# Kernel optimization log

Hardware: AMD Instinct MI355X
Metric: run time of the kernel (lower is better)

The kernel has to match this reference:

```python
import jax, jax.numpy as jnp
import numpy as np

NUM_CODES = 8192
LATENT_DIM = 256
BETA = 0.25
EPS_NORM = 1e-12  # F.normalize eps


def setup_inputs() -> dict:
    key = jax.random.key(0)
    k1, k2 = jax.random.split(key)
    z = jax.random.normal(k1, (8, LATENT_DIM, 32, 32), dtype=jnp.float32)
    # embedding initialized uniform(-1/K, 1/K); use that scale for realism
    codebook = jax.random.uniform(k2, (NUM_CODES, LATENT_DIM), dtype=jnp.float32,
                                  minval=-1.0 / NUM_CODES, maxval=1.0 / NUM_CODES)
    return {"z": z, "codebook": codebook}


def reference(z, codebook):
    # forward re-normalizes the codebook rows (F.normalize dim=1)
    norm = jnp.sqrt(jnp.sum(codebook * codebook, axis=1, keepdims=True))
    w = codebook / jnp.maximum(norm, EPS_NORM)                      # [K, D]

    z_perm = jnp.transpose(z, (0, 2, 3, 1))                          # [B, H, W, D]
    B, H, W, D = z_perm.shape
    zf = z_perm.reshape(-1, D)                                       # [N, D]

    # squared euclidean distances: ||z||^2 + ||w||^2 - 2 z w^T
    d = (jnp.sum(zf * zf, axis=1, keepdims=True)
         + jnp.sum(w * w, axis=1)
         - 2.0 * jnp.einsum('nd,kd->nk', zf, w))                     # [N, K]
    idx = jnp.argmin(d, axis=1)                                      # [N] int

    z_q = w[idx].reshape(B, H, W, D)                                 # gather

    # commitment + codebook loss
    loss = (jnp.mean((jax.lax.stop_gradient(z_q) - z_perm) ** 2)
            + BETA * jnp.mean((z_q - jax.lax.stop_gradient(z_perm)) ** 2))

    # straight-through estimator
    z_q = z_perm + jax.lax.stop_gradient(z_q - z_perm)

    # perplexity from codeword usage histogram (== mean of one-hots)
    N = idx.shape[0]
    counts = jnp.zeros((NUM_CODES,), dtype=jnp.float32).at[idx].add(1.0)
    avg_probs = counts / N
    perplexity = jnp.exp(-jnp.sum(avg_probs * jnp.log(avg_probs + 1e-10)))

    z_q = jnp.transpose(z_q, (0, 3, 1, 2))                           # back to NCHW
    return (z_q, idx, loss, perplexity)
```

## Files before the change

kernel.cpp:

```cpp
#include <hip/hip_runtime.h>
#include <hip/hip_bf16.h>
#include <math.h>

#define KC 8192
#define DD 256
#define NP 8192
#define ZQ_ELEMS 2097152
#define MARGIN_S 2.5e-4f
#define NPART 32

#define OFF_ABIG 0u
#define OFF_BBIG 8388608u
#define OFF_NRM  16777216u
#define OFF_WSQ  16809984u
#define OFF_ZSQ  16842752u
#define OFF_PV1  16875520u
#define OFF_PV2  17924096u
#define OFF_PK1  18972672u
#define OFF_LOSSP 20021248u
#define OFF_IDX  20025344u
#define OFF_FLAG 20058112u
#define OFF_HIST 20090880u
#define OFF_PACK 20123648u
#define OFF_LIST 20189184u
#define OFF_NFLG 20221952u

typedef __attribute__((ext_vector_type(8))) short bf16x8;
typedef __attribute__((ext_vector_type(4))) float f32x4;
typedef __attribute__((address_space(3))) void as3_void;
typedef const __attribute__((address_space(1))) void as1_cvoid;

#define GLOAD16(g, l) __builtin_amdgcn_global_load_lds((as1_cvoid*)(g), (as3_void*)(l), 16, 0, 0)

__device__ inline double waveReduceD(double v) {
#pragma unroll
    for (int off = 32; off; off >>= 1) v += __shfl_down(v, off, 64);
    return v;
}

static __device__ inline unsigned short f2bf(float f) {
    __hip_bfloat16 h = __float2bfloat16(f);
    return *(unsigned short*)&h;
}
static __device__ inline float bf2f(unsigned short u) {
    unsigned v = ((unsigned)u) << 16;
    float f;
    __builtin_memcpy(&f, &v, 4);
    return f;
}

__global__ __launch_bounds__(256) void prep(
    const float* __restrict__ cb, const float* __restrict__ z,
    unsigned short* __restrict__ Bbig, unsigned short* __restrict__ Abig,
    float* __restrict__ nrm, float* __restrict__ wsq, float* __restrict__ zsq,
    int* __restrict__ hist, int* __restrict__ nflag) {
    __shared__ double lred[4];
    __shared__ float mh;
    int bid = blockIdx.x, t = threadIdx.x;
    int lane = t & 63, wid = t >> 6;
    if (bid < KC) {
        int k = bid;
        if (k < 32) hist[k * 256 + t] = 0;
        if (k == 32 && t == 0) *nflag = 0;
        float c = cb[k * DD + t];
        double s = waveReduceD((double)c * (double)c);
        if (lane == 0) lred[wid] = s;
        __syncthreads();
        if (t == 0) {
            double tot = lred[0] + lred[1] + lred[2] + lred[3];
            float nf = sqrtf((float)tot);
            mh = fmaxf(nf, 1e-12f);
        }
        __syncthreads();
        float wv = c / mh;
        unsigned short hi = f2bf(wv);
        unsigned short lo = f2bf(wv - bf2f(hi));
        Bbig[k * 512 + t] = hi;
        Bbig[k * 512 + 256 + t] = lo;
        if (t == 0) nrm[k] = mh;
        __syncthreads();
        double s2 = waveReduceD((double)wv * (double)wv);
        if (lane == 0) lred[wid] = s2;
        __syncthreads();
        if (t == 0) wsq[k] = (float)(lred[0] + lred[1] + lred[2] + lred[3]);
    } else {
        int n = bid - KC;
        int b = n >> 10, hw = n & 1023;
        float v = z[(b * DD + t) * 1024 + hw];
        unsigned short hi = f2bf(v);
        unsigned short lo = f2bf(v - bf2f(hi));
        Abig[n * 512 + t] = hi;
        Abig[n * 512 + 256 + t] = lo;
        double s = waveReduceD((double)v * (double)v);
        if (lane == 0) lred[wid] = s;
        __syncthreads();
        if (t == 0) zsq[n] = (float)(lred[0] + lred[1] + lred[2] + lred[3]);
    }
}

__global__ __launch_bounds__(512, 2) void gemm_top2(
    const unsigned short* __restrict__ Abig, const unsigned short* __restrict__ Bbig,
    const float* __restrict__ wsq,
    float* __restrict__ pv1, float* __restrict__ pv2, int* __restrict__ pk1) {
    __shared__ unsigned short sAB[65536];

    int t = threadIdx.x;
    int l = t & 63, w = t >> 6;
    int wm = w >> 2, wn = w & 3;
    int kc0 = blockIdx.y * 256;
    int n0 = blockIdx.x * 256;

    int row0 = t >> 2;
    int lsw = (((t & 3) ^ ((row0 >> 1) & 3)) << 3);
    int subsw = (((l >> 4) ^ ((l >> 1) & 3)) << 3);

#define STAGE(kt_) do {                                                        \
    int p_ = (kt_) >> 3;                                                       \
    int zo_ = (p_ == 2 ? 256 : 0) + ((kt_) & 7) * 32;                          \
    int wo_ = (p_ == 1 ? 256 : 0) + ((kt_) & 7) * 32;                          \
    int b_ = ((kt_) & 3) * 16384;                                              \
    GLOAD16(Bbig + (size_t)(kc0 + row0) * 512 + wo_ + lsw, &sAB[b_ + t * 8]);  \
    GLOAD16(Bbig + (size_t)(kc0 + row0 + 128) * 512 + wo_ + lsw, &sAB[b_ + 4096 + t * 8]); \
    GLOAD16(Abig + (size_t)(n0 + row0) * 512 + zo_ + lsw, &sAB[b_ + 8192 + t * 8]); \
    GLOAD16(Abig + (size_t)(n0 + row0 + 128) * 512 + zo_ + lsw, &sAB[b_ + 12288 + t * 8]); \
} while (0)

    f32x4 acc[8][4];
#pragma unroll
    for (int mf = 0; mf < 8; ++mf) {
#pragma unroll
        for (int r = 0; r < 4; ++r) {
            float hv = -0.5f * wsq[kc0 + wm * 128 + mf * 16 + ((l >> 4) << 2) + r];
#pragma unroll
            for (int nf = 0; nf < 4; ++nf) acc[mf][nf][r] = hv;
        }
    }

#define KBODY(bufbase) do {                                                    \
    bf16x8 af[8], bfr[4];                                                      \
    _Pragma("unroll")                                                          \
    for (int mf = 0; mf < 8; ++mf)                                             \
        af[mf] = *(const bf16x8*)&sAB[(bufbase) + (wm * 128 + mf * 16 + (l & 15)) * 32 + subsw]; \
    _Pragma("unroll")                                                          \
    for (int nf = 0; nf < 4; ++nf)                                             \
        bfr[nf] = *(const bf16x8*)&sAB[(bufbase) + 8192 + (wn * 64 + nf * 16 + (l & 15)) * 32 + subsw]; \
    __builtin_amdgcn_s_setprio(1);                                             \
    _Pragma("unroll")                                                          \
    for (int mf = 0; mf < 8; ++mf)                                             \
        _Pragma("unroll")                                                      \
        for (int nf = 0; nf < 4; ++nf)                                         \
            acc[mf][nf] = __builtin_amdgcn_mfma_f32_16x16x32_bf16(af[mf], bfr[nf], acc[mf][nf], 0, 0, 0); \
    __builtin_amdgcn_s_setprio(0);                                             \
} while (0)

    STAGE(0);
    STAGE(1);
    STAGE(2);
    asm volatile("s_waitcnt vmcnt(8)" ::: "memory");
    __builtin_amdgcn_s_barrier();
    asm volatile("" ::: "memory");

    for (int kt = 0; kt < 21; ++kt) {
        STAGE(kt + 3);
        KBODY((kt & 3) * 16384);
        asm volatile("s_waitcnt vmcnt(8)" ::: "memory");
        __builtin_amdgcn_s_barrier();
        asm volatile("" ::: "memory");
    }
    KBODY(1 * 16384);
    asm volatile("s_waitcnt vmcnt(4)" ::: "memory");
    __builtin_amdgcn_s_barrier();
    asm volatile("" ::: "memory");
    KBODY(2 * 16384);
    asm volatile("s_waitcnt vmcnt(0)" ::: "memory");
    __builtin_amdgcn_s_barrier();
    asm volatile("" ::: "memory");
    KBODY(3 * 16384);

    float v1[4], v2[4];
    int k1[4];
#pragma unroll
    for (int nf = 0; nf < 4; ++nf) { v1[nf] = 3.4e38f; v2[nf] = 3.4e38f; k1[nf] = 0; }
#pragma unroll
    for (int mf = 0; mf < 8; ++mf) {
#pragma unroll
        for (int r = 0; r < 4; ++r) {
            int code = kc0 + wm * 128 + mf * 16 + ((l >> 4) << 2) + r;
#pragma unroll
            for (int nf = 0; nf < 4; ++nf) {
                float dv = -acc[mf][nf][r];
                bool lt = dv < v1[nf];
                v2[nf] = fminf(v2[nf], fmaxf(v1[nf], dv));
                v1[nf] = fminf(v1[nf], dv);
                k1[nf] = lt ? code : k1[nf];
            }
        }
    }
#pragma unroll
    for (int nf = 0; nf < 4; ++nf) {
#pragma unroll
        for (int mask = 16; mask <= 32; mask <<= 1) {
            float ov1 = __shfl_xor(v1[nf], mask, 64);
            float ov2 = __shfl_xor(v2[nf], mask, 64);
            int ok1 = __shfl_xor(k1[nf], mask, 64);
            bool take = (ov1 < v1[nf]) || (ov1 == v1[nf] && ok1 < k1[nf]);
            if (take) { v2[nf] = fminf(v1[nf], ov2); v1[nf] = ov1; k1[nf] = ok1; }
            else v2[nf] = fminf(v2[nf], ov1);
        }
    }
    __syncthreads();
    float* sv1 = (float*)sAB;
    float* sv2 = sv1 + 512;
    int* sk1 = (int*)(sv2 + 512);
    if ((l >> 4) == 0) {
#pragma unroll
        for (int nf = 0; nf < 4; ++nf) {
            int col = wn * 64 + nf * 16 + l;
            sv1[col * 2 + wm] = v1[nf];
            sv2[col * 2 + wm] = v2[nf];
            sk1[col * 2 + wm] = k1[nf];
        }
    }
    __syncthreads();
    if (t < 256) {
        float a1 = sv1[t * 2], b1 = sv1[t * 2 + 1];
        float a2 = sv2[t * 2], b2 = sv2[t * 2 + 1];
        int ak = sk1[t * 2], bk = sk1[t * 2 + 1];
        bool tb = (b1 < a1) || (b1 == a1 && bk < ak);
        float w1 = tb ? b1 : a1;
        int wk = tb ? bk : ak;
        float w2 = tb ? fminf(b2, a1) : fminf(a2, b1);
        pv1[blockIdx.y * NP + n0 + t] = w1;
        pv2[blockIdx.y * NP + n0 + t] = w2;
        pk1[blockIdx.y * NP + n0 + t] = wk;
    }
#undef STAGE
#undef KBODY
}

__global__ __launch_bounds__(256) void merge_top2(
    const float* __restrict__ pv1, const float* __restrict__ pv2,
    const int* __restrict__ pk1, int* __restrict__ idxw, int* __restrict__ flag,
    int* __restrict__ list, int* __restrict__ nflag,
    unsigned long long* __restrict__ packed) {
    int n = blockIdx.x * 256 + threadIdx.x;
    float gv1 = 3.4e38f, gv2 = 3.4e38f;
    int gk1 = 0;
#pragma unroll
    for (int ct = 0; ct < NPART; ++ct) {
        float v1 = pv1[ct * NP + n];
        if (v1 < gv1) {
            gv2 = fminf(gv1, pv2[ct * NP + n]);
            gv1 = v1;
            gk1 = pk1[ct * NP + n];
        } else {
            gv2 = fminf(gv2, v1);
        }
    }
    idxw[n] = gk1;
    int f = (gv2 - gv1 < MARGIN_S) ? 1 : 0;
    flag[n] = f;
    if (f) {
        packed[n] = 0xFFFFFFFFFFFFFFFFull;
        int pos = atomicAdd(nflag, 1);
        list[pos] = n;
    }
}

__global__ __launch_bounds__(256) void rescore_par(
    const float* __restrict__ z, const float* __restrict__ cb,
    const float* __restrict__ nrm, const float* __restrict__ wsq,
    const float* __restrict__ zsq, const int* __restrict__ list,
    const int* __restrict__ nflag, unsigned long long* __restrict__ packed) {
    __shared__ float sz[256];
    int nf = *nflag;
    int t = threadIdx.x;
    int lane = t & 63, wv = t >> 6;
    for (int ii = blockIdx.x; ii < nf; ii += 64) {
        int n = list[ii];
        int b = n >> 10, hw = n & 1023;
        __syncthreads();
        sz[t] = z[(b * DD + t) * 1024 + hw];
        __syncthreads();
        float4 zr = ((const float4*)sz)[lane];
        float zq = zsq[n];
        unsigned long long best = 0xFFFFFFFFFFFFFFFFull;
        int kbase = blockIdx.y * 256 + wv * 64;
        for (int j = 0; j < 64; ++j) {
            int k = kbase + j;
            float4 cc = *(const float4*)&cb[(size_t)k * DD + lane * 4];
            float p = (zr.x * cc.x + zr.y * cc.y) + (zr.z * cc.z + zr.w * cc.w);
#pragma unroll
            for (int off = 32; off; off >>= 1) p += __shfl_xor(p, off, 64);
            float dot = p / nrm[k];
            float dv = (zq + wsq[k]) - 2.0f * dot;
            unsigned bits = __float_as_uint(dv);
            bits = (bits & 0x80000000u) ? ~bits : (bits | 0x80000000u);
            unsigned long long pk = ((unsigned long long)bits << 32) | (unsigned)k;
            best = best < pk ? best : pk;
        }
        if (lane == 0) atomicMin(packed + n, best);
    }
}

__global__ __launch_bounds__(256) void fix_hist(
    const int* __restrict__ flag, const unsigned long long* __restrict__ packed,
    int* __restrict__ idxw, float* __restrict__ out, int* __restrict__ hist) {
    int n = blockIdx.x * 256 + threadIdx.x;
    int k = flag[n] ? (int)(packed[n] & 0xFFFFFFFFull) : idxw[n];
    idxw[n] = k;
    out[ZQ_ELEMS + n] = (float)k;
    atomicAdd(&hist[k], 1);
}

__global__ __launch_bounds__(256) void gather_loss(
    const float* __restrict__ z, const float* __restrict__ cb,
    const float* __restrict__ nrm, const int* __restrict__ idxw,
    float* __restrict__ out, double* __restrict__ lossp) {
    __shared__ double lred[4];
    int t = threadIdx.x;
    int base = (blockIdx.x * 256 + t) * 16;
    double s = 0.0;
#pragma unroll
    for (int q = 0; q < 4; ++q) {
        int e = base + q * 4;
        int b = e >> 18, d = (e >> 10) & 255, hw = e & 1023;
        int n = (b << 10) + hw;
        float4 zv = *(const float4*)&z[e];
        float o[4];
#pragma unroll
        for (int j = 0; j < 4; ++j) {
            int k = idxw[n + j];
            o[j] = cb[k * DD + d] / nrm[k];
        }
        *(float4*)&out[e] = make_float4(o[0], o[1], o[2], o[3]);
        float d0 = o[0] - zv.x, d1 = o[1] - zv.y, d2 = o[2] - zv.z, d3 = o[3] - zv.w;
        s += (double)(d0 * d0) + (double)(d1 * d1) + (double)(d2 * d2) + (double)(d3 * d3);
    }
    s = waveReduceD(s);
    int lane = t & 63, wid = t >> 6;
    if (lane == 0) lred[wid] = s;
    __syncthreads();
    if (t == 0) lossp[blockIdx.x] = lred[0] + lred[1] + lred[2] + lred[3];
}

__global__ __launch_bounds__(256) void finalize_kernel(
    const int* __restrict__ hist, const double* __restrict__ lossp,
    float* __restrict__ out) {
    __shared__ double lred[4];
    __shared__ double lsum;
    int t = threadIdx.x;
    int lane = t & 63, wid = t >> 6;
    double ls = lossp[t] + lossp[t + 256];
    ls = waveReduceD(ls);
    if (lane == 0) lred[wid] = ls;
    __syncthreads();
    if (t == 0) lsum = lred[0] + lred[1] + lred[2] + lred[3];
    __syncthreads();
    double s = 0.0;
    for (int i = t; i < KC; i += 256) {
        float p = (float)hist[i] * (1.0f / 8192.0f);
        float lg = logf(p + 1e-10f);
        s += (double)(p * lg);
    }
    s = waveReduceD(s);
    if (lane == 0) lred[wid] = s;
    __syncthreads();
    if (t == 0) {
        double tot = lred[0] + lred[1] + lred[2] + lred[3];
        float m = (float)(lsum / (double)ZQ_ELEMS);
        out[ZQ_ELEMS + NP] = m + 0.25f * m;
        out[ZQ_ELEMS + NP + 1] = expf(-(float)tot);
    }
}

extern "C" void kernel_launch(void* const* d_in, const int* in_sizes, int n_in,
                              void* d_out, int out_size, void* d_ws, size_t ws_size,
                              hipStream_t stream) {
    const float* z = (const float*)d_in[0];
    const float* cb = (const float*)d_in[1];
    float* out = (float*)d_out;
    char* ws = (char*)d_ws;

    unsigned short* Abig = (unsigned short*)(ws + OFF_ABIG);
    unsigned short* Bbig = (unsigned short*)(ws + OFF_BBIG);
    float* nrm = (float*)(ws + OFF_NRM);
    float* wsq = (float*)(ws + OFF_WSQ);
    float* zsq = (float*)(ws + OFF_ZSQ);
    float* pv1 = (float*)(ws + OFF_PV1);
    float* pv2 = (float*)(ws + OFF_PV2);
    int* pk1 = (int*)(ws + OFF_PK1);
    int* idxw = (int*)(ws + OFF_IDX);
    int* flag = (int*)(ws + OFF_FLAG);
    int* hist = (int*)(ws + OFF_HIST);
    double* lossp = (double*)(ws + OFF_LOSSP);
    unsigned long long* packed = (unsigned long long*)(ws + OFF_PACK);
    int* list = (int*)(ws + OFF_LIST);
    int* nflag = (int*)(ws + OFF_NFLG);

    prep<<<2 * KC, 256, 0, stream>>>(cb, z, Bbig, Abig, nrm, wsq, zsq, hist, nflag);
    gemm_top2<<<dim3(32, NPART), 512, 0, stream>>>(Abig, Bbig, wsq, pv1, pv2, pk1);
    merge_top2<<<NP / 256, 256, 0, stream>>>(pv1, pv2, pk1, idxw, flag, list, nflag, packed);
    rescore_par<<<dim3(64, 32), 256, 0, stream>>>(z, cb, nrm, wsq, zsq, list, nflag, packed);
    fix_hist<<<NP / 256, 256, 0, stream>>>(flag, packed, idxw, out, hist);
    gather_loss<<<ZQ_ELEMS / (256 * 16), 256, 0, stream>>>(z, cb, nrm, idxw, out, lossp);
    finalize_kernel<<<1, 256, 0, stream>>>(hist, lossp, out);
}
```

Measured before the change: 217.4 us.

## Switch GEMM to 32x32x16 MFMA, drop fix_hist kernel, simplify prep reductions

The GEMM moves from 16x16x32 to 32x32x16 bf16 MFMA tiles with a new LDS swizzle, which cuts LDS fragment reads per MFMA and simplifies the top-2 cross-lane reduction. The fix_hist kernel is removed: merge_top2 writes the final index into the packed array, and gather_loss emits the indices and histogram atomics. Prep no longer does a second reduction for wsq (it is derived from the norm) and no longer computes zsq, which rescore now computes on the fly. This saves a launch and some reduction passes, but wsq now comes from tot/mh² rather than an explicit sum, which could shift values slightly.

```diff
diff --git a/kernel.cpp b/kernel.cpp
--- a/kernel.cpp
+++ b/kernel.cpp
@@ -13,20 +13,17 @@
 #define OFF_BBIG 8388608u
 #define OFF_NRM  16777216u
 #define OFF_WSQ  16809984u
-#define OFF_ZSQ  16842752u
 #define OFF_PV1  16875520u
 #define OFF_PV2  17924096u
 #define OFF_PK1  18972672u
 #define OFF_LOSSP 20021248u
-#define OFF_IDX  20025344u
-#define OFF_FLAG 20058112u
 #define OFF_HIST 20090880u
 #define OFF_PACK 20123648u
 #define OFF_LIST 20189184u
 #define OFF_NFLG 20221952u
 
 typedef __attribute__((ext_vector_type(8))) short bf16x8;
-typedef __attribute__((ext_vector_type(4))) float f32x4;
+typedef __attribute__((ext_vector_type(16))) float f32x16;
 typedef __attribute__((address_space(3))) void as3_void;
 typedef const __attribute__((address_space(1))) void as1_cvoid;
 
@@ -52,7 +49,7 @@
 __global__ __launch_bounds__(256) void prep(
     const float* __restrict__ cb, const float* __restrict__ z,
     unsigned short* __restrict__ Bbig, unsigned short* __restrict__ Abig,
-    float* __restrict__ nrm, float* __restrict__ wsq, float* __restrict__ zsq,
+    float* __restrict__ nrm, float* __restrict__ wsq,
     int* __restrict__ hist, int* __restrict__ nflag) {
     __shared__ double lred[4];
     __shared__ float mh;
@@ -70,6 +67,8 @@
             double tot = lred[0] + lred[1] + lred[2] + lred[3];
             float nf = sqrtf((float)tot);
             mh = fmaxf(nf, 1e-12f);
+            nrm[k] = mh;
+            wsq[k] = (float)(tot / ((double)mh * (double)mh));
         }
         __syncthreads();
         float wv = c / mh;
@@ -77,12 +76,6 @@
         unsigned short lo = f2bf(wv - bf2f(hi));
         Bbig[k * 512 + t] = hi;
         Bbig[k * 512 + 256 + t] = lo;
-        if (t == 0) nrm[k] = mh;
-        __syncthreads();
-        double s2 = waveReduceD((double)wv * (double)wv);
-        if (lane == 0) lred[wid] = s2;
-        __syncthreads();
-        if (t == 0) wsq[k] = (float)(lred[0] + lred[1] + lred[2] + lred[3]);
     } else {
         int n = bid - KC;
         int b = n >> 10, hw = n & 1023;
@@ -91,10 +84,6 @@
         unsigned short lo = f2bf(v - bf2f(hi));
         Abig[n * 512 + t] = hi;
         Abig[n * 512 + 256 + t] = lo;
-        double s = waveReduceD((double)v * (double)v);
-        if (lane == 0) lred[wid] = s;
-        __syncthreads();
-        if (t == 0) zsq[n] = (float)(lred[0] + lred[1] + lred[2] + lred[3]);
     }
 }
 
@@ -107,61 +96,77 @@
     int t = threadIdx.x;
     int l = t & 63, w = t >> 6;
     int wm = w >> 2, wn = w & 3;
+    int l31 = l & 31, lhi = l >> 5;
     int kc0 = blockIdx.y * 256;
     int n0 = blockIdx.x * 256;
 
     int row0 = t >> 2;
-    int lsw = (((t & 3) ^ ((row0 >> 1) & 3)) << 3);
-    int subsw = (((l >> 4) ^ ((l >> 1) & 3)) << 3);
-
-#define STAGE(kt_) do {                                                        \
+    int fr = ((row0 >> 1) ^ (row0 >> 3)) & 3;
+    int kk = (((t & 3) ^ fr) << 3);
+    int flr = ((l31 >> 1) ^ (l31 >> 3)) & 3;
+
+#define STAGE4(kt_) do {                                                       \
     int p_ = (kt_) >> 3;                                                       \
     int zo_ = (p_ == 2 ? 256 : 0) + ((kt_) & 7) * 32;                          \
     int wo_ = (p_ == 1 ? 256 : 0) + ((kt_) & 7) * 32;                          \
     int b_ = ((kt_) & 3) * 16384;                                              \
-    GLOAD16(Bbig + (size_t)(kc0 + row0) * 512 + wo_ + lsw, &sAB[b_ + t * 8]);  \
-    GLOAD16(Bbig + (size_t)(kc0 + row0 + 128) * 512 + wo_ + lsw, &sAB[b_ + 4096 + t * 8]); \
-    GLOAD16(Abig + (size_t)(n0 + row0) * 512 + zo_ + lsw, &sAB[b_ + 8192 + t * 8]); \
-    GLOAD16(Abig + (size_t)(n0 + row0 + 128) * 512 + zo_ + lsw, &sAB[b_ + 12288 + t * 8]); \
+    GLOAD16(Bbig + (size_t)(kc0 + row0) * 512 + wo_ + kk, &sAB[b_ + t * 8]);   \
+    GLOAD16(Bbig + (size_t)(kc0 + row0 + 128) * 512 + wo_ + kk, &sAB[b_ + 4096 + t * 8]); \
+    GLOAD16(Abig + (size_t)(n0 + row0) * 512 + zo_ + kk, &sAB[b_ + 8192 + t * 8]); \
+    GLOAD16(Abig + (size_t)(n0 + row0 + 128) * 512 + zo_ + kk, &sAB[b_ + 12288 + t * 8]); \
 } while (0)
 
-    f32x4 acc[8][4];
-#pragma unroll
-    for (int mf = 0; mf < 8; ++mf) {
-#pragma unroll
-        for (int r = 0; r < 4; ++r) {
-            float hv = -0.5f * wsq[kc0 + wm * 128 + mf * 16 + ((l >> 4) << 2) + r];
-#pragma unroll
-            for (int nf = 0; nf < 4; ++nf) acc[mf][nf][r] = hv;
-        }
-    }
-
-#define KBODY(bufbase) do {                                                    \
-    bf16x8 af[8], bfr[4];                                                      \
+    f32x16 acc[4][2];
+#pragma unroll
+    for (int mt = 0; mt < 4; ++mt) {
+#pragma unroll
+        for (int r = 0; r < 16; ++r) {
+            float hv = -0.5f * wsq[kc0 + wm * 128 + mt * 32 + (r & 3) + 8 * (r >> 2) + 4 * lhi];
+            acc[mt][0][r] = hv;
+            acc[mt][1][r] = hv;
+        }
+    }
+
+    int aoff0 = (((0 + lhi) ^ flr) << 3);
+    int aoff1 = (((2 + lhi) ^ flr) << 3);
+
+#define KBODY(bb_) do {                                                        \
+    bf16x8 a0_[4], a1_[4], b0_[2], b1_[2];                                     \
     _Pragma("unroll")                                                          \
-    for (int mf = 0; mf < 8; ++mf)                                             \
-        af[mf] = *(const bf16x8*)&sAB[(bufbase) + (wm * 128 + mf * 16 + (l & 15)) * 32 + subsw]; \
+    for (int mt = 0; mt < 4; ++mt) {                                           \
+        int rb_ = (bb_) + (wm * 128 + mt * 32 + l31) * 32;                     \
+        a0_[mt] = *(const bf16x8*)&sAB[rb_ + aoff0];                           \
+        a1_[mt] = *(const bf16x8*)&sAB[rb_ + aoff1];                           \
+    }                                                                          \
     _Pragma("unroll")                                                          \
-    for (int nf = 0; nf < 4; ++nf)                                             \
-        bfr[nf] = *(const bf16x8*)&sAB[(bufbase) + 8192 + (wn * 64 + nf * 16 + (l & 15)) * 32 + subsw]; \
+    for (int nt = 0; nt < 2; ++nt) {                                           \
+        int rb_ = (bb_) + 8192 + (wn * 64 + nt * 32 + l31) * 32;               \
+        b0_[nt] = *(const bf16x8*)&sAB[rb_ + aoff0];                           \
+        b1_[nt] = *(const bf16x8*)&sAB[rb_ + aoff1];                           \
+    }                                                                          \
     __builtin_amdgcn_s_setprio(1);                                             \
     _Pragma("unroll")                                                          \
-    for (int mf = 0; mf < 8; ++mf)                                             \
+    for (int mt = 0; mt < 4; ++mt)                                             \
         _Pragma("unroll")                                                      \
-        for (int nf = 0; nf < 4; ++nf)                                         \
-            acc[mf][nf] = __builtin_amdgcn_mfma_f32_16x16x32_bf16(af[mf], bfr[nf], acc[mf][nf], 0, 0, 0); \
+        for (int nt = 0; nt < 2; ++nt)                                         \
+            acc[mt][nt] = __builtin_amdgcn_mfma_f32_32x32x16_bf16(a0_[mt], b0_[nt], acc[mt][nt], 0, 0, 0); \
+    _Pragma("unroll")                                                          \
+    for (int mt = 0; mt < 4; ++mt)                                             \
+        _Pragma("unroll")                                                      \
+        for (int nt = 0; nt < 2; ++nt)                                         \
+            acc[mt][nt] = __builtin_amdgcn_mfma_f32_32x32x16_bf16(a1_[mt], b1_[nt], acc[mt][nt], 0, 0, 0); \
     __builtin_amdgcn_s_setprio(0);                                             \
 } while (0)
 
-    STAGE(0);
-    STAGE(1);
-    STAGE(2);
+    STAGE4(0);
+    STAGE4(1);
+    STAGE4(2);
     asm volatile("s_waitcnt vmcnt(8)" ::: "memory");
     __builtin_amdgcn_s_barrier();
     asm volatile("" ::: "memory");
 
     for (int kt = 0; kt < 21; ++kt) {
-        STAGE(kt + 3);
+        STAGE4(kt + 3);
         KBODY((kt & 3) * 16384);
         asm volatile("s_waitcnt vmcnt(8)" ::: "memory");
         __builtin_amdgcn_s_barrier();
@@ -177,48 +182,45 @@
     asm volatile("" ::: "memory");
     KBODY(3 * 16384);
 
-    float v1[4], v2[4];
-    int k1[4];
-#pragma unroll
-    for (int nf = 0; nf < 4; ++nf) { v1[nf] = 3.4e38f; v2[nf] = 3.4e38f; k1[nf] = 0; }
-#pragma unroll
-    for (int mf = 0; mf < 8; ++mf) {
-#pragma unroll
-        for (int r = 0; r < 4; ++r) {
-            int code = kc0 + wm * 128 + mf * 16 + ((l >> 4) << 2) + r;
-#pragma unroll
-            for (int nf = 0; nf < 4; ++nf) {
-                float dv = -acc[mf][nf][r];
-                bool lt = dv < v1[nf];
-                v2[nf] = fminf(v2[nf], fmaxf(v1[nf], dv));
-                v1[nf] = fminf(v1[nf], dv);
-                k1[nf] = lt ? code : k1[nf];
+    float v1[2], v2[2];
+    int k1[2];
+#pragma unroll
+    for (int nt = 0; nt < 2; ++nt) { v1[nt] = 3.4e38f; v2[nt] = 3.4e38f; k1[nt] = 0; }
+#pragma unroll
+    for (int mt = 0; mt < 4; ++mt) {
+#pragma unroll
+        for (int r = 0; r < 16; ++r) {
+            int code = kc0 + wm * 128 + mt * 32 + (r & 3) + 8 * (r >> 2) + 4 * lhi;
+#pragma unroll
+            for (int nt = 0; nt < 2; ++nt) {
+                float dv = -acc[mt][nt][r];
+                bool lt = dv < v1[nt];
+                v2[nt] = fminf(v2[nt], fmaxf(v1[nt], dv));
+                v1[nt] = fminf(v1[nt], dv);
+                k1[nt] = lt ? code : k1[nt];
             }
         }
     }
 #pragma unroll
-    for (int nf = 0; nf < 4; ++nf) {
-#pragma unroll
-        for (int mask = 16; mask <= 32; mask <<= 1) {
-            float ov1 = __shfl_xor(v1[nf], mask, 64);
-            float ov2 = __shfl_xor(v2[nf], mask, 64);
-            int ok1 = __shfl_xor(k1[nf], mask, 64);
-            bool take = (ov1 < v1[nf]) || (ov1 == v1[nf] && ok1 < k1[nf]);
-            if (take) { v2[nf] = fminf(v1[nf], ov2); v1[nf] = ov1; k1[nf] = ok1; }
-            else v2[nf] = fminf(v2[nf], ov1);
-        }
+    for (int nt = 0; nt < 2; ++nt) {
+        float ov1 = __shfl_xor(v1[nt], 32, 64);
+        float ov2 = __shfl_xor(v2[nt], 32, 64);
+        int ok1 = __shfl_xor(k1[nt], 32, 64);
+        bool take = (ov1 < v1[nt]) || (ov1 == v1[nt] && ok1 < k1[nt]);
+        if (take) { v2[nt] = fminf(v1[nt], ov2); v1[nt] = ov1; k1[nt] = ok1; }
+        else v2[nt] = fminf(v2[nt], ov1);
     }
     __syncthreads();
     float* sv1 = (float*)sAB;
     float* sv2 = sv1 + 512;
     int* sk1 = (int*)(sv2 + 512);
-    if ((l >> 4) == 0) {
-#pragma unroll
-        for (int nf = 0; nf < 4; ++nf) {
-            int col = wn * 64 + nf * 16 + l;
-            sv1[col * 2 + wm] = v1[nf];
-            sv2[col * 2 + wm] = v2[nf];
-            sk1[col * 2 + wm] = k1[nf];
+    if (lhi == 0) {
+#pragma unroll
+        for (int nt = 0; nt < 2; ++nt) {
+            int col = wn * 64 + nt * 32 + l31;
+            sv1[col * 2 + wm] = v1[nt];
+            sv2[col * 2 + wm] = v2[nt];
+            sk1[col * 2 + wm] = k1[nt];
         }
     }
     __syncthreads();
@@ -234,14 +236,13 @@
         pv2[blockIdx.y * NP + n0 + t] = w2;
         pk1[blockIdx.y * NP + n0 + t] = wk;
     }
-#undef STAGE
+#undef STAGE4
 #undef KBODY
 }
 
 __global__ __launch_bounds__(256) void merge_top2(
     const float* __restrict__ pv1, const float* __restrict__ pv2,
-    const int* __restrict__ pk1, int* __restrict__ idxw, int* __restrict__ flag,
-    int* __restrict__ list, int* __restrict__ nflag,
+    const int* __restrict__ pk1, int* __restrict__ list, int* __restrict__ nflag,
     unsigned long long* __restrict__ packed) {
     int n = blockIdx.x * 256 + threadIdx.x;
     float gv1 = 3.4e38f, gv2 = 3.4e38f;
@@ -257,11 +258,9 @@
             gv2 = fminf(gv2, v1);
         }
     }
-    idxw[n] = gk1;
     int f = (gv2 - gv1 < MARGIN_S) ? 1 : 0;
-    flag[n] = f;
+    packed[n] = f ? 0xFFFFFFFFFFFFFFFFull : (unsigned long long)(unsigned)gk1;
     if (f) {
-        packed[n] = 0xFFFFFFFFFFFFFFFFull;
         int pos = atomicAdd(nflag, 1);
         list[pos] = n;
     }
@@ -270,8 +269,8 @@
 __global__ __launch_bounds__(256) void rescore_par(
     const float* __restrict__ z, const float* __restrict__ cb,
     const float* __restrict__ nrm, const float* __restrict__ wsq,
-    const float* __restrict__ zsq, const int* __restrict__ list,
-    const int* __restrict__ nflag, unsigned long long* __restrict__ packed) {
+    const int* __restrict__ list, const int* __restrict__ nflag,
+    unsigned long long* __restrict__ packed) {
     __shared__ float sz[256];
     int nf = *nflag;
     int t = threadIdx.x;
@@ -283,7 +282,11 @@
         sz[t] = z[(b * DD + t) * 1024 + hw];
         __syncthreads();
         float4 zr = ((const float4*)sz)[lane];
-        float zq = zsq[n];
+        double zqd = (double)zr.x * zr.x + (double)zr.y * zr.y
+                   + (double)zr.z * zr.z + (double)zr.w * zr.w;
+#pragma unroll
+        for (int off = 32; off; off >>= 1) zqd += __shfl_xor(zqd, off, 64);
+        float zq = (float)zqd;
         unsigned long long best = 0xFFFFFFFFFFFFFFFFull;
         int kbase = blockIdx.y * 256 + wv * 64;
         for (int j = 0; j < 64; ++j) {
@@ -303,20 +306,10 @@
     }
 }
 
-__global__ __launch_bounds__(256) void fix_hist(
-    const int* __restrict__ flag, const unsigned long long* __restrict__ packed,
-    int* __restrict__ idxw, float* __restrict__ out, int* __restrict__ hist) {
-    int n = blockIdx.x * 256 + threadIdx.x;
-    int k = flag[n] ? (int)(packed[n] & 0xFFFFFFFFull) : idxw[n];
-    idxw[n] = k;
-    out[ZQ_ELEMS + n] = (float)k;
-    atomicAdd(&hist[k], 1);
-}
-
 __global__ __launch_bounds__(256) void gather_loss(
     const float* __restrict__ z, const float* __restrict__ cb,
-    const float* __restrict__ nrm, const int* __restrict__ idxw,
-    float* __restrict__ out, double* __restrict__ lossp) {
+    const float* __restrict__ nrm, const unsigned long long* __restrict__ packed,
+    float* __restrict__ out, double* __restrict__ lossp, int* __restrict__ hist) {
     __shared__ double lred[4];
     int t = threadIdx.x;
     int base = (blockIdx.x * 256 + t) * 16;
@@ -328,12 +321,20 @@
         int n = (b << 10) + hw;
         float4 zv = *(const float4*)&z[e];
         float o[4];
+        int ks[4];
 #pragma unroll
         for (int j = 0; j < 4; ++j) {
-            int k = idxw[n + j];
-            o[j] = cb[k * DD + d] / nrm[k];
+            ks[j] = (int)(packed[n + j] & 0xFFFFFFFFull);
+            o[j] = cb[ks[j] * DD + d] / nrm[ks[j]];
         }
         *(float4*)&out[e] = make_float4(o[0], o[1], o[2], o[3]);
+        if (d == 0) {
+#pragma unroll
+            for (int j = 0; j < 4; ++j) {
+                out[ZQ_ELEMS + n + j] = (float)ks[j];
+                atomicAdd(&hist[ks[j]], 1);
+            }
+        }
         float d0 = o[0] - zv.x, d1 = o[1] - zv.y, d2 = o[2] - zv.z, d3 = o[3] - zv.w;
         s += (double)(d0 * d0) + (double)(d1 * d1) + (double)(d2 * d2) + (double)(d3 * d3);
     }
@@ -386,23 +387,19 @@
     unsigned short* Bbig = (unsigned short*)(ws + OFF_BBIG);
     float* nrm = (float*)(ws + OFF_NRM);
     float* wsq = (float*)(ws + OFF_WSQ);
-    float* zsq = (float*)(ws + OFF_ZSQ);
     float* pv1 = (float*)(ws + OFF_PV1);
     float* pv2 = (float*)(ws + OFF_PV2);
     int* pk1 = (int*)(ws + OFF_PK1);
-    int* idxw = (int*)(ws + OFF_IDX);
-    int* flag = (int*)(ws + OFF_FLAG);
     int* hist = (int*)(ws + OFF_HIST);
     double* lossp = (double*)(ws + OFF_LOSSP);
     unsigned long long* packed = (unsigned long long*)(ws + OFF_PACK);
     int* list = (int*)(ws + OFF_LIST);
     int* nflag = (int*)(ws + OFF_NFLG);
 
-    prep<<<2 * KC, 256, 0, stream>>>(cb, z, Bbig, Abig, nrm, wsq, zsq, hist, nflag);
+    prep<<<2 * KC, 256, 0, stream>>>(cb, z, Bbig, Abig, nrm, wsq, hist, nflag);
     gemm_top2<<<dim3(32, NPART), 512, 0, stream>>>(Abig, Bbig, wsq, pv1, pv2, pk1);
-    merge_top2<<<NP / 256, 256, 0, stream>>>(pv1, pv2, pk1, idxw, flag, list, nflag, packed);
-    rescore_par<<<dim3(64, 32), 256, 0, stream>>>(z, cb, nrm, wsq, zsq, list, nflag, packed);
-    fix_hist<<<NP / 256, 256, 0, stream>>>(flag, packed, idxw, out, hist);
-    gather_loss<<<ZQ_ELEMS / (256 * 16), 256, 0, stream>>>(z, cb, nrm, idxw, out, lossp);
+    merge_top2<<<NP / 256, 256, 0, stream>>>(pv1, pv2, pk1, list, nflag, packed);
+    rescore_par<<<dim3(64, 32), 256, 0, stream>>>(z, cb, nrm, wsq, list, nflag, packed);
+    gather_loss<<<ZQ_ELEMS / (256 * 16), 256, 0, stream>>>(z, cb, nrm, packed, out, lossp, hist);
     finalize_kernel<<<1, 256, 0, stream>>>(hist, lossp, out);
 }
```

Result: slower. 226.6 us (+4.2%).
